# Optimization experiments

Hardware: AMD Instinct MI355X
Metric: run time of the kernel (lower is better)

Reference implementation:

```python
import jax, jax.numpy as jnp
import numpy as np

LUMINANCE_Q = np.array([
    [16, 11, 10, 16, 24, 40, 51, 61],
    [12, 12, 14, 19, 26, 58, 60, 55],
    [14, 13, 16, 24, 40, 57, 69, 56],
    [14, 17, 22, 29, 51, 87, 80, 62],
    [18, 22, 37, 56, 68, 109, 103, 77],
    [24, 36, 55, 64, 81, 104, 113, 92],
    [49, 64, 78, 87, 103, 121, 120, 101],
    [72, 92, 95, 98, 112, 100, 103, 99]], dtype=np.float64) / 100.0

def _dct_matrix():
    # C[k, n] = grid_factors[k] * cos(pi*k*(2n+1)/16); grid_factors = 2*[1/sqrt(32), 1/sqrt(16)x7]
    k = np.arange(8)[:, None]
    n = np.arange(8)[None, :]
    a = np.full(8, 2.0 / np.sqrt(2 * 8))
    a[0] = 2.0 / np.sqrt(4 * 8)
    C = a[:, None] * np.cos(np.pi * k * (2 * n + 1) / 16.0)
    return jnp.asarray(C, dtype=jnp.float32)

DCT_C = _dct_matrix()
Q_TABLE = jnp.asarray(LUMINANCE_Q, dtype=jnp.float32)

def setup_inputs() -> dict:
    key = jax.random.key(0)
    k1, k2 = jax.random.split(key)
    B, H, W = 16, 1024, 1024
    # pixel-like values around 128
    image = 128.0 + 40.0 * jax.random.normal(k1, (B, 1, H, W), dtype=jnp.float32)
    quality_factor = jax.random.randint(k2, (B,), 1, 100).astype(jnp.float32)
    return {"image": image, "quality_factor": quality_factor}

def reference(image, quality_factor):
    B, _, H, W = image.shape
    # Set_QF: factor per batch element, shape [B,1,1,1,1]
    factor = jnp.where(quality_factor < 50.0,
                       5000.0 / quality_factor,
                       200.0 - 2.0 * quality_factor).reshape(B, 1, 1, 1, 1)
    # Image_2_Blocks: [B, H/8, 8, W/8, 8] -> [B, 8, 8, H/8, W/8], then center
    blocks = image.reshape(B, H // 8, 8, W // 8, 8).transpose(0, 2, 4, 1, 3) - 128.0
    # 2D orthonormal DCT-II over the two 8-wide in-block axes (axes 1 then 2)
    dct = jnp.einsum('un,vm,bnmij->buvij', DCT_C, DCT_C, blocks)
    out = dct / (factor * Q_TABLE[None, :, :, None, None])
    # quantize=False: no rounding
    return out.reshape(B, 64, H // 8, W // 8)
```

## Files before the change

### kernel.cpp

```cpp
#include <hip/hip_runtime.h>
#include <cstddef>


static constexpr double LUMQ[64] = {
    16, 11, 10, 16, 24, 40, 51, 61,
    12, 12, 14, 19, 26, 58, 60, 55,
    14, 13, 16, 24, 40, 57, 69, 56,
    14, 17, 22, 29, 51, 87, 80, 62,
    18, 22, 37, 56, 68, 109, 103, 77,
    24, 36, 55, 64, 81, 104, 113, 92,
    49, 64, 78, 87, 103, 121, 120, 101,
    72, 92, 95, 98, 112, 100, 103, 99,
};

static constexpr double AANS[8] = {
    1.0, 1.3870398453221475, 1.3065629648763766, 1.1758756024193588,
    1.0, 0.7856949583871022, 0.5411961001461970, 0.2758993792829430,
};

__device__ __host__ __forceinline__ constexpr float outScale(int u, int v) {
    return (float)(100.0 / (LUMQ[u * 8 + v] * 8.0 * AANS[u] * AANS[v]));
}

__device__ __forceinline__ void aan_dct8(float& x0, float& x1, float& x2,
                                         float& x3, float& x4, float& x5,
                                         float& x6, float& x7) {
    const float t0 = x0 + x7, t7 = x0 - x7;
    const float t1 = x1 + x6, t6 = x1 - x6;
    const float t2 = x2 + x5, t5 = x2 - x5;
    const float t3 = x3 + x4, t4 = x3 - x4;

    float t10 = t0 + t3;
    const float t13 = t0 - t3;
    const float t11 = t1 + t2;
    const float t12 = t1 - t2;
    x0 = t10 + t11;
    x4 = t10 - t11;
    const float z1 = (t12 + t13) * 0.70710678118654752f;
    x2 = t13 + z1;
    x6 = t13 - z1;

    t10 = t4 + t5;
    const float u11 = t5 + t6;
    const float u12 = t6 + t7;
    const float z5 = (t10 - u12) * 0.38268343236508977f;
    const float z2 = 0.54119610014619698f * t10 + z5;
    const float z4 = 1.30656296487637653f * u12 + z5;
    const float z3 = u11 * 0.70710678118654752f;
    const float z11 = t7 + z3;
    const float z13 = t7 - z3;
    x5 = z13 + z2;
    x3 = z13 - z2;
    x1 = z11 + z4;
    x7 = z11 - z4;
}

__global__ __launch_bounds__(256) void jpeg_dct_quant_kernel(
    const float* __restrict__ img,
    const float* __restrict__ qfv,
    float* __restrict__ out)
{
    const int bid = blockIdx.x * 256 + threadIdx.x;
    const int j = bid & 127;
    const int i = (bid >> 7) & 127;
    const int b = bid >> 14;

    const float* src = img + ((size_t)b << 20) + (size_t)(i * 8) * 1024 + j * 8;

    float m[8][8];
    #pragma unroll
    for (int n = 0; n < 8; ++n) {
        const float4 r0 = *reinterpret_cast<const float4*>(src + (size_t)n * 1024);
        const float4 r1 = *reinterpret_cast<const float4*>(src + (size_t)n * 1024 + 4);
        m[n][0] = r0.x; m[n][1] = r0.y; m[n][2] = r0.z; m[n][3] = r0.w;
        m[n][4] = r1.x; m[n][5] = r1.y; m[n][6] = r1.z; m[n][7] = r1.w;
    }

    #pragma unroll
    for (int n = 0; n < 8; ++n)
        aan_dct8(m[n][0], m[n][1], m[n][2], m[n][3],
                 m[n][4], m[n][5], m[n][6], m[n][7]);

    #pragma unroll
    for (int v = 0; v < 8; ++v)
        aan_dct8(m[0][v], m[1][v], m[2][v], m[3][v],
                 m[4][v], m[5][v], m[6][v], m[7][v]);

    m[0][0] -= 8192.0f;

    const float qf = qfv[b];
    const float factor = (qf < 50.0f) ? (5000.0f / qf) : (200.0f - 2.0f * qf);
    const float invf = 1.0f / factor;

    float* dst = out + ((size_t)b << 20) + (size_t)i * 128 + j;
    #pragma unroll
    for (int u = 0; u < 8; ++u)
        #pragma unroll
        for (int v = 0; v < 8; ++v)
            dst[(size_t)(u * 8 + v) * 16384] = m[u][v] * (invf * outScale(u, v));
}

extern "C" void kernel_launch(void* const* d_in, const int* in_sizes, int n_in,
                              void* d_out, int out_size, void* d_ws, size_t ws_size,
                              hipStream_t stream) {
    const float* img = (const float*)d_in[0];
    const float* qfv = (const float*)d_in[1];
    float* out = (float*)d_out;

    jpeg_dct_quant_kernel<<<1024, 256, 0, stream>>>(img, qfv, out);
}
```

Baseline: 111.5 us.

## Stage DCT outputs through LDS to emit coalesced float4 stores

```diff
diff --git a/kernel.cpp b/kernel.cpp
--- a/kernel.cpp
+++ b/kernel.cpp
@@ -60,12 +60,17 @@
     const float* __restrict__ qfv,
     float* __restrict__ out)
 {
-    const int bid = blockIdx.x * 256 + threadIdx.x;
+    __shared__ float lds[32 * 256];
+
+    const int tid = threadIdx.x;
+    const int wg = blockIdx.x;
+    const int bid = wg * 256 + tid;
     const int j = bid & 127;
-    const int i = (bid >> 7) & 127;
+    const int irow = bid >> 7;
     const int b = bid >> 14;
 
-    const float* src = img + ((size_t)b << 20) + (size_t)(i * 8) * 1024 + j * 8;
+    const float* src = img + ((size_t)b << 20)
+                     + (size_t)((irow & 127) * 8) * 1024 + j * 8;
 
     float m[8][8];
     #pragma unroll
@@ -92,12 +97,38 @@
     const float factor = (qf < 50.0f) ? (5000.0f / qf) : (200.0f - 2.0f * qf);
     const float invf = 1.0f / factor;
 
-    float* dst = out + ((size_t)b << 20) + (size_t)i * 128 + j;
     #pragma unroll
     for (int u = 0; u < 8; ++u)
         #pragma unroll
         for (int v = 0; v < 8; ++v)
-            dst[(size_t)(u * 8 + v) * 16384] = m[u][v] * (invf * outScale(u, v));
+            m[u][v] *= invf * outScale(u, v);
+
+    const int a  = tid >> 7;
+    const int w  = tid >> 6;
+    const int l  = tid & 63;
+    const int i0 = (wg << 1) & 127;
+
+    float* dstbase = out + ((size_t)b << 20) + (size_t)i0 * 128 + (l << 2);
+
+    #pragma unroll
+    for (int phase = 0; phase < 2; ++phase) {
+        if (phase) __syncthreads();
+
+        #pragma unroll
+        for (int u = phase * 4; u < phase * 4 + 4; ++u)
+            #pragma unroll
+            for (int v = 0; v < 8; ++v)
+                lds[(u * 8 + v - phase * 32) * 256 + a * 128 + j] = m[u][v];
+        __syncthreads();
+
+        #pragma unroll
+        for (int k = 0; k < 8; ++k) {
+            const int cl = w * 8 + k;
+            const int c  = phase * 32 + cl;
+            *reinterpret_cast<float4*>(dstbase + (size_t)c * 16384) =
+                *reinterpret_cast<const float4*>(&lds[cl * 256 + (l << 2)]);
+        }
+    }
 }
 
 extern "C" void kernel_launch(void* const* d_in, const int* in_sizes, int n_in,
```

New measurement: 112.0 us. Within noise of the previous version (+0.5%).
